# Performance work log

Measured on AMD Instinct MI355X. Metric: run time of the kernel, lower is better.

## Reference

```python
import jax, jax.numpy as jnp
import numpy as np

EMB = 1024
HEADS = 16
HEAD_DIM = EMB // HEADS
EPS = 1e-5


def setup_inputs() -> dict:
    key = jax.random.key(0)
    ks = jax.random.split(key, 10)
    B, T, D = 2, 2048, EMB
    s = 1.0 / np.sqrt(D)
    inp = {
        "x": jax.random.normal(ks[0], (B, T, D), dtype=jnp.float32),
        "wq": jax.random.normal(ks[1], (D, D), dtype=jnp.float32) * s,
        "bq": jnp.zeros((D,), jnp.float32),
        "wk": jax.random.normal(ks[2], (D, D), dtype=jnp.float32) * s,
        "bk": jnp.zeros((D,), jnp.float32),
        "wv": jax.random.normal(ks[3], (D, D), dtype=jnp.float32) * s,
        "bv": jnp.zeros((D,), jnp.float32),
        "wo": jax.random.normal(ks[4], (D, D), dtype=jnp.float32) * s,
        "bo": jnp.zeros((D,), jnp.float32),
        "gamma": jnp.ones((D,), jnp.float32),
        "beta": jnp.zeros((D,), jnp.float32),
    }
    return inp


def _attention(x, wq, bq, wk, bk, wv, bv, wo, bo, gamma, beta):
    B, T, D = x.shape
    H, Hd = HEADS, HEAD_DIM
    q = (x @ wq + bq).reshape(B, T, H, Hd)
    k = (x @ wk + bk).reshape(B, T, H, Hd)
    v = (x @ wv + bv).reshape(B, T, H, Hd)
    # scores: [B, H, T, T]
    scores = jnp.einsum("bthd,bshd->bhts", q, k) / np.sqrt(Hd)
    attn = jax.nn.softmax(scores, axis=-1)  # dropout is identity in eval
    ctx = jnp.einsum("bhts,bshd->bthd", attn, v).reshape(B, T, D)
    out = ctx @ wo + bo
    y = x + out  # residual (dropout identity)
    mu = jnp.mean(y, axis=-1, keepdims=True)
    var = jnp.var(y, axis=-1, keepdims=True)
    return (y - mu) * jax.lax.rsqrt(var + EPS) * gamma + beta


def reference(x, wq, bq, wk, bk, wv, bv, wo, bo, gamma, beta):
    return _attention(x, wq, bq, wk, bk, wv, bv, wo, bo, gamma, beta)
```

## Files before the change

kernel.cpp:

```cpp
#include <hip/hip_runtime.h>

#define BSZ   2
#define TSEQ  2048
#define DMOD  1024
#define NHEAD 16
#define HDIM  64
#define MROW  (BSZ*TSEQ)
#define LNEPS 1e-5f
#define QSCALE 0.18033688011f

typedef __bf16 bf16x8 __attribute__((ext_vector_type(8)));
typedef float  f32x4  __attribute__((ext_vector_type(4)));
typedef unsigned short us8 __attribute__((ext_vector_type(8)));
typedef unsigned short us4 __attribute__((ext_vector_type(4)));

__device__ __forceinline__ unsigned short f2bf(float f) {
    unsigned u = __float_as_uint(f);
    u += 0x7FFF + ((u >> 16) & 1);
    return (unsigned short)(u >> 16);
}
__device__ __forceinline__ float bf2f(unsigned short u) {
    return __uint_as_float((unsigned)u << 16);
}

__device__ __forceinline__ float fexp2(float x) {
#if __has_builtin(__builtin_amdgcn_exp2f)
    return __builtin_amdgcn_exp2f(x);
#else
    return __expf(x * 0.6931471805599453f);
#endif
}

__device__ __forceinline__ void gld_lds16(const void* g, void* l) {
    __builtin_amdgcn_global_load_lds(
        (const __attribute__((address_space(1))) unsigned int*)g,
        (__attribute__((address_space(3))) unsigned int*)l, 16, 0, 0);
}

__global__ __launch_bounds__(256) void prep_k(
    const float* __restrict__ x,
    const float* __restrict__ wq, const float* __restrict__ wk,
    const float* __restrict__ wv, const float* __restrict__ wo,
    unsigned short* __restrict__ Xb,
    unsigned short* __restrict__ WqkvT, unsigned short* __restrict__ WoT)
{
    const int tid = threadIdx.x;
    if (blockIdx.x < 2048) {
        const size_t i = ((size_t)blockIdx.x * 256 + tid) * 8;
        float4 a = *(const float4*)&x[i];
        float4 b = *(const float4*)&x[i + 4];
        union { unsigned short u[8]; uint4 v; } o;
        o.u[0]=f2bf(a.x); o.u[1]=f2bf(a.y); o.u[2]=f2bf(a.z); o.u[3]=f2bf(a.w);
        o.u[4]=f2bf(b.x); o.u[5]=f2bf(b.y); o.u[6]=f2bf(b.z); o.u[7]=f2bf(b.w);
        *(uint4*)&Xb[i] = o.v;
        return;
    }
    __shared__ float T[64][68];
    const int id = blockIdx.x - 2048;
    const int z  = id >> 8;
    const int bx = id & 15;
    const int by = (id >> 4) & 15;
    const float* W = (z == 0) ? wq : (z == 1) ? wk : (z == 2) ? wv : wo;
    unsigned short* Wt = (z < 3) ? (WqkvT + (size_t)z*1024*1024) : WoT;
    const int lr = tid >> 4, lc = (tid & 15) * 4;
    #pragma unroll
    for (int p = 0; p < 4; ++p) {
        const int kk = p*16 + lr;
        float4 v = *(const float4*)&W[(size_t)(by*64 + kk)*1024 + bx*64 + lc];
        T[lc+0][kk] = v.x; T[lc+1][kk] = v.y; T[lc+2][kk] = v.z; T[lc+3][kk] = v.w;
    }
    __syncthreads();
    #pragma unroll
    for (int p = 0; p < 2; ++p) {
        const int nl = p*32 + (tid >> 3);
        const int kb = (tid & 7) * 8;
        float4 a = *(const float4*)&T[nl][kb];
        float4 b = *(const float4*)&T[nl][kb+4];
        union { unsigned short u[8]; uint4 v; } o;
        o.u[0]=f2bf(a.x); o.u[1]=f2bf(a.y); o.u[2]=f2bf(a.z); o.u[3]=f2bf(a.w);
        o.u[4]=f2bf(b.x); o.u[5]=f2bf(b.y); o.u[6]=f2bf(b.z); o.u[7]=f2bf(b.w);
        *(uint4*)&Wt[(size_t)(bx*64 + nl)*1024 + by*64 + kb] = o.v;
    }
}


#define PH_SYNC() do { __builtin_amdgcn_s_barrier(); \
    asm volatile("s_waitcnt lgkmcnt(0)" ::: "memory"); \
    __builtin_amdgcn_sched_barrier(0); } while (0)

template<int N>
__device__ __forceinline__ void vmwait() {
    if constexpr (N == 0)      asm volatile("s_waitcnt vmcnt(0)" ::: "memory");
    else if constexpr (N == 2) asm volatile("s_waitcnt vmcnt(2)" ::: "memory");
    else if constexpr (N == 3) asm volatile("s_waitcnt vmcnt(3)" ::: "memory");
    else                       asm volatile("s_waitcnt vmcnt(4)" ::: "memory");
}

template<int NB>
struct CoreT {
    const unsigned short *sA, *sB;
    unsigned short *A0w, *A1w, *B0w, *B1w;
    const unsigned short *fA0, *fA1, *fB0, *fB1;
    int swz0, swz1;
};

__device__ __forceinline__ void stageA4(const unsigned short* s, unsigned short* d) {
    #pragma unroll
    for (int u = 0; u < 4; ++u) gld_lds16(s + u*64*1024, d + u*4096);
}
template<int NB>
__device__ __forceinline__ void stageBall(const unsigned short* s, unsigned short* d) {
    #pragma unroll
    for (int u = 0; u < NB; ++u) gld_lds16(s + u*64*1024, d + u*4096);
}
__device__ __forceinline__ void stageB01(const unsigned short* s, unsigned short* d) {
    gld_lds16(s, d); gld_lds16(s + 64*1024, d + 4096);
}
template<int NB>
__device__ __forceinline__ void stageBrest(const unsigned short* s, unsigned short* d) {
    #pragma unroll
    for (int u = 2; u < NB; ++u) gld_lds16(s + u*64*1024, d + u*4096);
}

template<int NB>
__device__ __forceinline__ void core_setup(CoreT<NB>& C, unsigned short* LDS,
    const unsigned short* A, const unsigned short* Bt, int bm, int bn, int kbase)
{
    const int tid = threadIdx.x;
    const int w = tid >> 6, lane = tid & 63;
    const int quad = lane >> 4, l16 = lane & 15;
    const int wm = w >> 2, wn = w & 3;
    const int r_l = lane >> 3, c_l = lane & 7;
    C.sA = A  + (size_t)(bm + w*8 + r_l)*1024 + (c_l ^ r_l)*8 + kbase;
    C.sB = Bt + (size_t)(bn + w*8 + r_l)*1024 + (c_l ^ r_l)*8 + kbase;
    unsigned short* A0 = LDS;
    unsigned short* A1 = LDS + 16384;
    unsigned short* B0 = LDS + 32768;
    unsigned short* B1 = B0 + NB*4096;
    C.A0w = A0 + w*512; C.A1w = A1 + w*512;
    C.B0w = B0 + w*512; C.B1w = B1 + w*512;
    C.fA0 = A0 + (wm*128 + l16)*64; C.fA1 = A1 + (wm*128 + l16)*64;
    C.fB0 = B0 + (wn*NB*16 + l16)*64;  C.fB1 = B1 + (wn*NB*16 + l16)*64;
    C.swz0 = ( quad      ^ (l16 & 7)) * 8;
    C.swz1 = ((4 + quad) ^ (l16 & 7)) * 8;
}

template<int NB>
__device__ __forceinline__ void ld_b(const CoreT<NB>& C, bf16x8 (&bfr)[NB][2],
                                     const unsigned short* fB) {
    #pragma unroll
    for (int n = 0; n < NB; ++n) {
        bfr[n][0] = *(const bf16x8*)(fB + n*1024 + C.swz0);
        bfr[n][1] = *(const bf16x8*)(fB + n*1024 + C.swz1);
    }
}

template<int Q, int NB>
__device__ __forceinline__ void ld_a(const CoreT<NB>& C, bf16x8 (&af)[2][2],
                                     const unsigned short* fA) {
    #pragma unroll
    for (int dm = 0; dm < 2; ++dm) {
        af[dm][0] = *(const bf16x8*)(fA + (Q*2+dm)*1024 + C.swz0);
        af[dm][1] = *(const bf16x8*)(fA + (Q*2+dm)*1024 + C.swz1);
    }
}

template<int Q, int NB>
__device__ __forceinline__ void mma_q(f32x4 (&acc)[8][NB], bf16x8 (&af)[2][2],
                                      bf16x8 (&bfr)[NB][2]) {
    __builtin_amdgcn_s_setprio(1);
    #pragma unroll
    for (int dm = 0; dm < 2; ++dm)
        #pragma unroll
        for (int n = 0; n < NB; ++n) {
            f32x4 t = acc[Q*2+dm][n];
            t = __builtin_amdgcn_mfma_f32_16x16x32_bf16(af[dm][0], bfr[n][0], t, 0, 0, 0);
            t = __builtin_amdgcn_mfma_f32_16x16x32_bf16(af[dm][1], bfr[n][1], t, 0, 0, 0);
            acc[Q*2+dm][n] = t;
        }
    __builtin_amdgcn_s_setprio(0);
}

template<int NIT, int NB>
__device__ __forceinline__ void core_kloop(const CoreT<NB>& C, f32x4 (&acc)[8][NB])
{
    stageA4(C.sA, C.A0w);
    stageBall<NB>(C.sB,      C.B0w);
    stageBall<NB>(C.sB + 64, C.B1w);
    vmwait<NB>();
    __builtin_amdgcn_s_barrier();

    bf16x8 bfr[NB][2];
    bf16x8 af[2][2];

    #pragma unroll 1
    for (int it = 0; it < NIT - 1; ++it) {
        const int kk = it * 128;
        ld_b<NB>(C, bfr, C.fB0);
        ld_a<0,NB>(C, af, C.fA0);
        stageA4(C.sA + kk + 64, C.A1w);
        PH_SYNC();  mma_q<0,NB>(acc, af, bfr);
        __builtin_amdgcn_s_barrier();
        ld_a<1,NB>(C, af, C.fA0);
        stageB01(C.sB + kk + 128, C.B0w);
        PH_SYNC();  mma_q<1,NB>(acc, af, bfr);
        __builtin_amdgcn_s_barrier();
        ld_a<2,NB>(C, af, C.fA0);
        stageBrest<NB>(C.sB + kk + 128, C.B0w);
        PH_SYNC();  mma_q<2,NB>(acc, af, bfr);
        __builtin_amdgcn_s_barrier();
        ld_a<3,NB>(C, af, C.fA0);
        PH_SYNC();  mma_q<3,NB>(acc, af, bfr);
        vmwait<NB>();
        __builtin_amdgcn_s_barrier();
        ld_b<NB>(C, bfr, C.fB1);
        ld_a<0,NB>(C, af, C.fA1);
        stageA4(C.sA + kk + 128, C.A0w);
        PH_SYNC();  mma_q<0,NB>(acc, af, bfr);
        __builtin_amdgcn_s_barrier();
        ld_a<1,NB>(C, af, C.fA1);
        stageB01(C.sB + kk + 192, C.B1w);
        PH_SYNC();  mma_q<1,NB>(acc, af, bfr);
        __builtin_amdgcn_s_barrier();
        ld_a<2,NB>(C, af, C.fA1);
        stageBrest<NB>(C.sB + kk + 192, C.B1w);
        PH_SYNC();  mma_q<2,NB>(acc, af, bfr);
        __builtin_amdgcn_s_barrier();
        ld_a<3,NB>(C, af, C.fA1);
        PH_SYNC();  mma_q<3,NB>(acc, af, bfr);
        vmwait<NB>();
        __builtin_amdgcn_s_barrier();
    }

    {
        const int kk = (NIT - 1) * 128;
        ld_b<NB>(C, bfr, C.fB0);
        ld_a<0,NB>(C, af, C.fA0);
        stageA4(C.sA + kk + 64, C.A1w);
        PH_SYNC();  mma_q<0,NB>(acc, af, bfr);
        __builtin_amdgcn_s_barrier();
        ld_a<1,NB>(C, af, C.fA0); PH_SYNC(); mma_q<1,NB>(acc, af, bfr); __builtin_amdgcn_s_barrier();
        ld_a<2,NB>(C, af, C.fA0); PH_SYNC(); mma_q<2,NB>(acc, af, bfr); __builtin_amdgcn_s_barrier();
        ld_a<3,NB>(C, af, C.fA0); PH_SYNC(); mma_q<3,NB>(acc, af, bfr);
        vmwait<0>();
        __builtin_amdgcn_s_barrier();
        ld_b<NB>(C, bfr, C.fB1);
        ld_a<0,NB>(C, af, C.fA1); PH_SYNC(); mma_q<0,NB>(acc, af, bfr); __builtin_amdgcn_s_barrier();
        ld_a<1,NB>(C, af, C.fA1); PH_SYNC(); mma_q<1,NB>(acc, af, bfr); __builtin_amdgcn_s_barrier();
        ld_a<2,NB>(C, af, C.fA1); PH_SYNC(); mma_q<2,NB>(acc, af, bfr); __builtin_amdgcn_s_barrier();
        ld_a<3,NB>(C, af, C.fA1); PH_SYNC(); mma_q<3,NB>(acc, af, bfr);
    }
}

__global__ __launch_bounds__(512, 1) void gemm_qkv_k(
    const unsigned short* __restrict__ A, const unsigned short* __restrict__ Bt,
    const float* __restrict__ b0, const float* __restrict__ b1,
    const float* __restrict__ b2,
    unsigned short* __restrict__ oQ, unsigned short* __restrict__ oK,
    unsigned short* __restrict__ oV)
{
    extern __shared__ unsigned short LDS[];
    const int ob = blockIdx.x;
    const int wg = (ob & 7) * 24 + (ob >> 3);
    const int by = wg / 12, bx = wg - by*12;
    const int bm = by * 256, bn = bx * 256;

    CoreT<4> C;
    core_setup<4>(C, LDS, A, Bt, bm, bn, 0);

    f32x4 acc[8][4];
    #pragma unroll
    for (int i = 0; i < 8; ++i)
        #pragma unroll
        for (int j = 0; j < 4; ++j) acc[i][j] = (f32x4){0.f,0.f,0.f,0.f};

    core_kloop<8,4>(C, acc);

    const int tid = threadIdx.x;
    const int w = tid >> 6, lane = tid & 63;
    const int quad = lane >> 4, l16 = lane & 15;
    const int wm = w >> 2, wn = w & 3;
    const int seg = bn >> 10;
    const int cb  = bn & 1023;
    if (seg < 2) {
        unsigned short* O = (seg == 0) ? oQ : oK;
        const float sc = (seg == 0) ? QSCALE : 1.0f;
        const float* bias = (seg == 0) ? b0 : b1;
        #pragma unroll
        for (int n = 0; n < 4; ++n) {
            const int col = cb + wn*64 + n*16 + l16;
            const float bs = bias[col];
            #pragma unroll
            for (int m = 0; m < 8; ++m)
                #pragma unroll
                for (int r = 0; r < 4; ++r) {
                    const int grow = bm + wm*128 + m*16 + quad*4 + r;
                    O[(size_t)grow*1024 + col] = f2bf((acc[m][n][r] + bs) * sc);
                }
        }
    } else {
        #pragma unroll
        for (int n = 0; n < 4; ++n) {
            const int ch = cb + wn*64 + n*16 + l16;
            const float bs = b2[ch];
            #pragma unroll
            for (int m = 0; m < 8; ++m) {
                const int grow0 = bm + wm*128 + m*16 + quad*4;
                us4 o;
                #pragma unroll
                for (int r = 0; r < 4; ++r) o[r] = f2bf(acc[m][n][r] + bs);
                *(us4*)&oV[(size_t)ch*MROW + grow0] = o;
            }
        }
    }
}

__global__ __launch_bounds__(512, 2) void gemm_proj_k(
    const unsigned short* __restrict__ A, const unsigned short* __restrict__ Bt,
    unsigned short* __restrict__ P)
{
    extern __shared__ unsigned short LDS[];
    const int ob = blockIdx.x;
    const int wg = (ob & 7) * 16 + (ob >> 3);
    const int by = wg >> 3, bx = wg & 7;
    const int kz = blockIdx.y;
    const int bm = by * 256, bn = bx * 128;

    CoreT<2> C;
    core_setup<2>(C, LDS, A, Bt, bm, bn, kz * 512);

    f32x4 acc[8][2];
    #pragma unroll
    for (int i = 0; i < 8; ++i)
        #pragma unroll
        for (int j = 0; j < 2; ++j) acc[i][j] = (f32x4){0.f,0.f,0.f,0.f};

    core_kloop<4,2>(C, acc);

    const int tid = threadIdx.x;
    const int w = tid >> 6, lane = tid & 63;
    const int quad = lane >> 4, l16 = lane & 15;
    const int wm = w >> 2, wn = w & 3;
    unsigned short* O = P + (size_t)kz*MROW*1024;
    #pragma unroll
    for (int n = 0; n < 2; ++n) {
        const int col = bn + wn*32 + n*16 + l16;
        #pragma unroll
        for (int m = 0; m < 8; ++m)
            #pragma unroll
            for (int r = 0; r < 4; ++r) {
                const int grow = bm + wm*128 + m*16 + quad*4 + r;
                O[(size_t)grow*1024 + col] = f2bf(acc[m][n][r]);
            }
    }
}

__global__ __launch_bounds__(256, 4) void attn_k(
    const unsigned short* __restrict__ Qg,
    const unsigned short* __restrict__ Kg,
    const unsigned short* __restrict__ Vtg,
    unsigned short* __restrict__ CTX)
{
    extern __shared__ __align__(16) char lds_raw[];
    unsigned short* Ks = (unsigned short*)lds_raw;
    unsigned short* Vs = (unsigned short*)(lds_raw + 8192);
    unsigned short* Qs = (unsigned short*)lds_raw;
    float* Od = (float*)lds_raw;
    float* Ld = (float*)(lds_raw + 17408);

    const int tid  = threadIdx.x;
    const int wv   = tid >> 6;
    const int lane = tid & 63;
    const int quad = lane >> 4;
    const int l16  = lane & 15;
    const int wq   = wv & 1;
    const int wk   = wv >> 1;

    const int n    = blockIdx.x;
    const int slot = n >> 3;
    const int grp  = (n & 7) + 8 * (slot >> 5);
    const int qx   = slot & 31;
    const int h    = grp >> 1;
    const int b    = grp & 1;
    const int qb   = qx * 64;

    {
        const int r  = tid >> 2;
        const int cb = (tid & 3) * 16;
        const unsigned short* Qrow = Qg + ((size_t)(b*TSEQ + qb + r))*DMOD + h*HDIM + cb;
        *(us8*)&Qs[r*72 + cb]     = *(const us8*)&Qrow[0];
        *(us8*)&Qs[r*72 + cb + 8] = *(const us8*)&Qrow[8];
    }
    __syncthreads();
    bf16x8 qf[2][2];
    #pragma unroll
    for (int nt = 0; nt < 2; ++nt)
        #pragma unroll
        for (int kh = 0; kh < 2; ++kh)
            qf[nt][kh] = *(const bf16x8*)&Qs[(wq*32 + nt*16 + l16)*72 + kh*32 + quad*8];
    __syncthreads();

    const int sr = lane >> 3;
    const int sc = lane & 7;
    const bool isK = (wv < 2);
    const int part = wv & 1;
    const unsigned short* gbase;
    unsigned int goff[4];
    unsigned short* ldst;
    if (isK) {
        gbase = Kg + ((size_t)(b*TSEQ))*DMOD + h*HDIM;
        #pragma unroll
        for (int s = 0; s < 4; ++s) {
            const int R = part*32 + s*8 + sr;
            const int gc = sc ^ ((R ^ (R >> 2)) & 7);
            goff[s] = (unsigned)(R*DMOD + gc*8);
        }
        ldst = Ks + part*2048;
    } else {
        gbase = Vtg + ((size_t)(h*HDIM))*MROW + b*TSEQ;
        #pragma unroll
        for (int s = 0; s < 4; ++s) {
            const int D = part*32 + s*8 + sr;
            const int gc = sc ^ (D & 7);
            goff[s] = (unsigned)(D*MROW + gc*8);
        }
        ldst = Vs + part*2048;
    }
    const size_t gstep = isK ? (size_t)64*DMOD : (size_t)64;

    const int rowA_l = (l16 >> 2)*8 + (l16 & 3);
    const int rA = wk*32 + rowA_l;
    const int rB = rA + 4;
    const int swA = ((rA ^ (rA >> 2)) & 7);
    const int swB = ((rB ^ (rB >> 2)) & 7);
    const unsigned short* kA0 = &Ks[rA*64 + ( quad      ^ swA)*8];
    const unsigned short* kA1 = &Ks[rA*64 + ((4 + quad) ^ swA)*8];
    const unsigned short* kB0 = &Ks[rB*64 + ( quad      ^ swB)*8];
    const unsigned short* kB1 = &Ks[rB*64 + ((4 + quad) ^ swB)*8];
    const unsigned short* vp[4];
    #pragma unroll
    for (int dt = 0; dt < 4; ++dt)
        vp[dt] = &Vs[(dt*16 + l16)*64 + ((wk*4 + quad) ^ (l16 & 7))*8];

    bf16x8 onef;
    { union { unsigned short u[8]; bf16x8 v; } o1;
      #pragma unroll
      for (int i = 0; i < 8; ++i) o1.u[i] = 0x3F80;
      onef = o1.v; }

    f32x4 oacc[4][2];
    f32x4 lacc[2];
    #pragma unroll
    for (int dt = 0; dt < 4; ++dt)
        #pragma unroll
        for (int nt = 0; nt < 2; ++nt) oacc[dt][nt] = (f32x4){0.f,0.f,0.f,0.f};
    lacc[0] = (f32x4){0.f,0.f,0.f,0.f};
    lacc[1] = (f32x4){0.f,0.f,0.f,0.f};

    #pragma unroll 1
    for (int it = 0; it < 32; ++it) {
        __syncthreads();
        #pragma unroll
        for (int s = 0; s < 4; ++s)
            gld_lds16(gbase + (size_t)it*gstep + goff[s], ldst + s*512);
        __syncthreads();

        bf16x8 ka0 = *(const bf16x8*)kA0;
        bf16x8 ka1 = *(const bf16x8*)kA1;
        bf16x8 kb0 = *(const bf16x8*)kB0;
        bf16x8 kb1 = *(const bf16x8*)kB1;
        bf16x8 vf[4];
        #pragma unroll
        for (int dt = 0; dt < 4; ++dt) vf[dt] = *(const bf16x8*)vp[dt];

        bf16x8 pf[2];
        #pragma unroll
        for (int nt = 0; nt < 2; ++nt) {
            f32x4 z = (f32x4){0.f,0.f,0.f,0.f};
            z = __builtin_amdgcn_mfma_f32_16x16x32_bf16(ka0, qf[nt][0], z, 0, 0, 0);
            f32x4 sA = __builtin_amdgcn_mfma_f32_16x16x32_bf16(ka1, qf[nt][1], z, 0, 0, 0);
            f32x4 z2 = (f32x4){0.f,0.f,0.f,0.f};
            z2 = __builtin_amdgcn_mfma_f32_16x16x32_bf16(kb0, qf[nt][0], z2, 0, 0, 0);
            f32x4 sB = __builtin_amdgcn_mfma_f32_16x16x32_bf16(kb1, qf[nt][1], z2, 0, 0, 0);
            float eA[4], eB[4];
            #pragma unroll
            for (int r = 0; r < 4; ++r) { eA[r] = fexp2(sA[r]); eB[r] = fexp2(sB[r]); }
            union { unsigned d[4]; bf16x8 v; } up;
            up.d[0] = __builtin_amdgcn_perm(__float_as_uint(eA[1]), __float_as_uint(eA[0]), 0x07060302);
            up.d[1] = __builtin_amdgcn_perm(__float_as_uint(eA[3]), __float_as_uint(eA[2]), 0x07060302);
            up.d[2] = __builtin_amdgcn_perm(__float_as_uint(eB[1]), __float_as_uint(eB[0]), 0x07060302);
            up.d[3] = __builtin_amdgcn_perm(__float_as_uint(eB[3]), __float_as_uint(eB[2]), 0x07060302);
            pf[nt] = up.v;
        }
        __builtin_amdgcn_s_setprio(1);
        #pragma unroll
        for (int nt = 0; nt < 2; ++nt) {
            lacc[nt] = __builtin_amdgcn_mfma_f32_16x16x32_bf16(onef, pf[nt], lacc[nt], 0, 0, 0);
            #pragma unroll
            for (int dt = 0; dt < 4; ++dt)
                oacc[dt][nt] = __builtin_amdgcn_mfma_f32_16x16x32_bf16(vf[dt], pf[nt], oacc[dt][nt], 0, 0, 0);
        }
        __builtin_amdgcn_s_setprio(0);
    }

    __syncthreads();
    if (wk == 0) {
        float* od = Od + wq*32*68;
        #pragma unroll
        for (int nt = 0; nt < 2; ++nt) {
            #pragma unroll
            for (int dt = 0; dt < 4; ++dt)
                *(f32x4*)&od[(nt*16 + l16)*68 + dt*16 + quad*4] = oacc[dt][nt];
            if (quad == 0) Ld[wq*32 + nt*16 + l16] = lacc[nt][0];
        }
    }
    __syncthreads();
    if (wk == 1) {
        const float* od = Od + wq*32*68;
        #pragma unroll
        for (int nt = 0; nt < 2; ++nt) {
            const float l = Ld[wq*32 + nt*16 + l16] + lacc[nt][0];
            const float inv = 1.f / l;
            const int q = qb + wq*32 + nt*16 + l16;
            unsigned short* crow = CTX + ((size_t)(b*TSEQ + q))*DMOD + h*HDIM;
            #pragma unroll
            for (int dt = 0; dt < 4; ++dt) {
                f32x4 p = *(const f32x4*)&od[(nt*16 + l16)*68 + dt*16 + quad*4];
                us4 o;
                #pragma unroll
                for (int r = 0; r < 4; ++r) o[r] = f2bf((p[r] + oacc[dt][nt][r]) * inv);
                *(us4*)&crow[dt*16 + quad*4] = o;
            }
        }
    }
}

__global__ __launch_bounds__(256) void red_ln_k(
    const float* __restrict__ x, const unsigned short* __restrict__ P,
    const float* __restrict__ bo,
    const float* __restrict__ gamma, const float* __restrict__ beta,
    float* __restrict__ out)
{
    __shared__ float rs[4], rss[4];
    const int row = blockIdx.x;
    const int tid = threadIdx.x;
    const int c = tid * 4;
    const float4 xv = *(const float4*)&x[(size_t)row*DMOD + c];
    const us4 p0 = *(const us4*)&P[(size_t)row*DMOD + c];
    const us4 p1 = *(const us4*)&P[(size_t)(MROW + row)*DMOD + c];
    const float4 bv4 = *(const float4*)&bo[c];
    const float v0 = xv.x + bf2f(p0[0]) + bf2f(p1[0]) + bv4.x;
    const float v1 = xv.y + bf2f(p0[1]) + bf2f(p1[1]) + bv4.y;
    const float v2 = xv.z + bf2f(p0[2]) + bf2f(p1[2]) + bv4.z;
    const float v3 = xv.w + bf2f(p0[3]) + bf2f(p1[3]) + bv4.w;
    float s  = v0 + v1 + v2 + v3;
    float ss = v0*v0 + v1*v1 + v2*v2 + v3*v3;
    #pragma unroll
    for (int o = 32; o > 0; o >>= 1) {
        s  += __shfl_down(s,  o, 64);
        ss += __shfl_down(ss, o, 64);
    }
    if ((tid & 63) == 0) { rs[tid >> 6] = s; rss[tid >> 6] = ss; }
    __syncthreads();
    s  = rs[0] + rs[1] + rs[2] + rs[3];
    ss = rss[0] + rss[1] + rss[2] + rss[3];
    const float mean = s * (1.f/DMOD);
    const float var  = ss * (1.f/DMOD) - mean*mean;
    const float rstd = rsqrtf(var + LNEPS);
    const float4 gv = *(const float4*)&gamma[c];
    const float4 bv = *(const float4*)&beta[c];
    float4 o;
    o.x = (v0 - mean)*rstd*gv.x + bv.x;
    o.y = (v1 - mean)*rstd*gv.y + bv.y;
    o.z = (v2 - mean)*rstd*gv.z + bv.z;
    o.w = (v3 - mean)*rstd*gv.w + bv.w;
    *(float4*)&out[(size_t)row*DMOD + c] = o;
}

extern "C" void kernel_launch(void* const* d_in, const int* in_sizes, int n_in,
                              void* d_out, int out_size, void* d_ws, size_t ws_size,
                              hipStream_t stream) {
    const float* x     = (const float*)d_in[0];
    const float* wq    = (const float*)d_in[1];
    const float* bq    = (const float*)d_in[2];
    const float* wk    = (const float*)d_in[3];
    const float* bk    = (const float*)d_in[4];
    const float* wvp   = (const float*)d_in[5];
    const float* bvp   = (const float*)d_in[6];
    const float* wo    = (const float*)d_in[7];
    const float* bo    = (const float*)d_in[8];
    const float* gamma = (const float*)d_in[9];
    const float* beta  = (const float*)d_in[10];
    float* out = (float*)d_out;

    unsigned short* Xb    = (unsigned short*)d_ws;
    unsigned short* WqkvT = Xb    + (size_t)MROW*DMOD;
    unsigned short* WoT   = WqkvT + (size_t)3072*1024;
    unsigned short* Qb    = WoT   + (size_t)1024*1024;
    unsigned short* Kb    = Qb    + (size_t)MROW*DMOD;
    unsigned short* VtG   = Kb    + (size_t)MROW*DMOD;
    unsigned short* CTXb  = VtG   + (size_t)DMOD*MROW;
    unsigned short* Pp    = CTXb  + (size_t)MROW*DMOD;

    prep_k<<<3072, 256, 0, stream>>>(x, wq, wk, wvp, wo, Xb, WqkvT, WoT);

    gemm_qkv_k<<<dim3(192), 512, 131072, stream>>>(
        Xb, WqkvT, bq, bk, bvp, Qb, Kb, VtG);

    attn_k<<<dim3(1024), 256, 17664, stream>>>(Qb, Kb, VtG, CTXb);

    gemm_proj_k<<<dim3(128, 2), 512, 98304, stream>>>(CTXb, WoT, Pp);

    red_ln_k<<<MROW, 256, 0, stream>>>(x, Pp, bo, gamma, beta, out);
}
```

Measured before the change: 191.4 us.

## Retile QKV GEMM to 256x192 tiles and rebuild projection GEMM with 128x128 tiles

The QKV GEMM moves from 256x256 tiles over 192 blocks to 256x192 tiles over 256 blocks, so the block count better matches the 256 CUs. Because a 192-wide tile can now straddle the Q/K/V boundary, the epilogue picks the output segment for each 16-column fragment. The output-projection GEMM gets a new 4-wave core with 128x128 tiles and its own double-buffered staging schedule, launched as 512 blocks instead of 256. This raises occupancy and reduces tail imbalance, at the cost of less data reuse per tile and more global loads in total.

After: 191.6 us. No clear change (+0.1%).

```diff
diff --git a/kernel.cpp b/kernel.cpp
--- a/kernel.cpp
+++ b/kernel.cpp
@@ -261,34 +261,35 @@
 {
     extern __shared__ unsigned short LDS[];
     const int ob = blockIdx.x;
-    const int wg = (ob & 7) * 24 + (ob >> 3);
-    const int by = wg / 12, bx = wg - by*12;
-    const int bm = by * 256, bn = bx * 256;
-
-    CoreT<4> C;
-    core_setup<4>(C, LDS, A, Bt, bm, bn, 0);
-
-    f32x4 acc[8][4];
+    const int wg = (ob & 7) * 32 + (ob >> 3);
+    const int by = wg >> 4, bx = wg & 15;
+    const int bm = by * 256, bn = bx * 192;
+
+    CoreT<3> C;
+    core_setup<3>(C, LDS, A, Bt, bm, bn, 0);
+
+    f32x4 acc[8][3];
     #pragma unroll
     for (int i = 0; i < 8; ++i)
         #pragma unroll
-        for (int j = 0; j < 4; ++j) acc[i][j] = (f32x4){0.f,0.f,0.f,0.f};
-
-    core_kloop<8,4>(C, acc);
+        for (int j = 0; j < 3; ++j) acc[i][j] = (f32x4){0.f,0.f,0.f,0.f};
+
+    core_kloop<8,3>(C, acc);
 
     const int tid = threadIdx.x;
     const int w = tid >> 6, lane = tid & 63;
     const int quad = lane >> 4, l16 = lane & 15;
     const int wm = w >> 2, wn = w & 3;
-    const int seg = bn >> 10;
-    const int cb  = bn & 1023;
-    if (seg < 2) {
-        unsigned short* O = (seg == 0) ? oQ : oK;
-        const float sc = (seg == 0) ? QSCALE : 1.0f;
-        const float* bias = (seg == 0) ? b0 : b1;
-        #pragma unroll
-        for (int n = 0; n < 4; ++n) {
-            const int col = cb + wn*64 + n*16 + l16;
+    #pragma unroll
+    for (int n = 0; n < 3; ++n) {
+        const int c0  = bn + wn*48 + n*16;
+        const int seg = c0 >> 10;
+        const int cl0 = c0 & 1023;
+        if (seg < 2) {
+            unsigned short* O = (seg == 0) ? oQ : oK;
+            const float sc = (seg == 0) ? QSCALE : 1.0f;
+            const float* bias = (seg == 0) ? b0 : b1;
+            const int col = cl0 + l16;
             const float bs = bias[col];
             #pragma unroll
             for (int m = 0; m < 8; ++m)
@@ -297,11 +298,8 @@
                     const int grow = bm + wm*128 + m*16 + quad*4 + r;
                     O[(size_t)grow*1024 + col] = f2bf((acc[m][n][r] + bs) * sc);
                 }
-        }
-    } else {
-        #pragma unroll
-        for (int n = 0; n < 4; ++n) {
-            const int ch = cb + wn*64 + n*16 + l16;
+        } else {
+            const int ch = cl0 + l16;
             const float bs = b2[ch];
             #pragma unroll
             for (int m = 0; m < 8; ++m) {
@@ -315,41 +313,179 @@
     }
 }
 
-__global__ __launch_bounds__(512, 2) void gemm_proj_k(
-    const unsigned short* __restrict__ A, const unsigned short* __restrict__ Bt,
-    unsigned short* __restrict__ P)
-{
-    extern __shared__ unsigned short LDS[];
-    const int ob = blockIdx.x;
-    const int wg = (ob & 7) * 16 + (ob >> 3);
-    const int by = wg >> 3, bx = wg & 7;
-    const int kz = blockIdx.y;
-    const int bm = by * 256, bn = bx * 128;
-
-    CoreT<2> C;
-    core_setup<2>(C, LDS, A, Bt, bm, bn, kz * 512);
-
-    f32x4 acc[8][2];
-    #pragma unroll
-    for (int i = 0; i < 8; ++i)
-        #pragma unroll
-        for (int j = 0; j < 2; ++j) acc[i][j] = (f32x4){0.f,0.f,0.f,0.f};
-
-    core_kloop<4,2>(C, acc);
-
+struct CoreP {
+    const unsigned short *sA, *sB;
+    unsigned short *A0w, *A1w, *B0w, *B1w;
+    const unsigned short *fA0, *fA1, *fB0, *fB1;
+    int swz0, swz1;
+};
+
+__device__ __forceinline__ void stage4p(const unsigned short* s, unsigned short* d) {
+    #pragma unroll
+    for (int u = 0; u < 4; ++u) gld_lds16(s + u*32*1024, d + u*2048);
+}
+__device__ __forceinline__ void stage01p(const unsigned short* s, unsigned short* d) {
+    gld_lds16(s, d); gld_lds16(s + 32*1024, d + 2048);
+}
+__device__ __forceinline__ void stage23p(const unsigned short* s, unsigned short* d) {
+    gld_lds16(s + 2*32*1024, d + 2*2048); gld_lds16(s + 3*32*1024, d + 3*2048);
+}
+
+__device__ __forceinline__ void corep_setup(CoreP& C, unsigned short* LDS,
+    const unsigned short* A, const unsigned short* Bt, int bm, int bn, int kbase)
+{
     const int tid = threadIdx.x;
     const int w = tid >> 6, lane = tid & 63;
     const int quad = lane >> 4, l16 = lane & 15;
-    const int wm = w >> 2, wn = w & 3;
+    const int wm = w >> 1, wn = w & 1;
+    const int r_l = lane >> 3, c_l = lane & 7;
+    C.sA = A  + (size_t)(bm + w*8 + r_l)*1024 + (c_l ^ r_l)*8 + kbase;
+    C.sB = Bt + (size_t)(bn + w*8 + r_l)*1024 + (c_l ^ r_l)*8 + kbase;
+    unsigned short* A0 = LDS;
+    unsigned short* A1 = LDS + 8192;
+    unsigned short* B0 = LDS + 16384;
+    unsigned short* B1 = LDS + 24576;
+    C.A0w = A0 + w*512; C.A1w = A1 + w*512;
+    C.B0w = B0 + w*512; C.B1w = B1 + w*512;
+    C.fA0 = A0 + (wm*64 + l16)*64; C.fA1 = A1 + (wm*64 + l16)*64;
+    C.fB0 = B0 + (wn*64 + l16)*64; C.fB1 = B1 + (wn*64 + l16)*64;
+    C.swz0 = ( quad      ^ (l16 & 7)) * 8;
+    C.swz1 = ((4 + quad) ^ (l16 & 7)) * 8;
+}
+
+__device__ __forceinline__ void ld_bp(const CoreP& C, bf16x8 (&bfr)[4][2],
+                                      const unsigned short* fB) {
+    #pragma unroll
+    for (int n = 0; n < 4; ++n) {
+        bfr[n][0] = *(const bf16x8*)(fB + n*1024 + C.swz0);
+        bfr[n][1] = *(const bf16x8*)(fB + n*1024 + C.swz1);
+    }
+}
+template<int Q>
+__device__ __forceinline__ void ld_ap(const CoreP& C, bf16x8 (&af)[2],
+                                      const unsigned short* fA) {
+    af[0] = *(const bf16x8*)(fA + Q*1024 + C.swz0);
+    af[1] = *(const bf16x8*)(fA + Q*1024 + C.swz1);
+}
+template<int Q>
+__device__ __forceinline__ void mma_p(f32x4 (&acc)[4][4], bf16x8 (&af)[2],
+                                      bf16x8 (&bfr)[4][2]) {
+    __builtin_amdgcn_s_setprio(1);
+    #pragma unroll
+    for (int n = 0; n < 4; ++n) {
+        f32x4 t = acc[Q][n];
+        t = __builtin_amdgcn_mfma_f32_16x16x32_bf16(af[0], bfr[n][0], t, 0, 0, 0);
+        t = __builtin_amdgcn_mfma_f32_16x16x32_bf16(af[1], bfr[n][1], t, 0, 0, 0);
+        acc[Q][n] = t;
+    }
+    __builtin_amdgcn_s_setprio(0);
+}
+
+template<int NIT>
+__device__ __forceinline__ void corep_kloop(const CoreP& C, f32x4 (&acc)[4][4])
+{
+    stage4p(C.sA, C.A0w);
+    stage4p(C.sB, C.B0w);
+    stage4p(C.sB + 64, C.B1w);
+    vmwait<4>();
+    __builtin_amdgcn_s_barrier();
+
+    bf16x8 bfr[4][2];
+    bf16x8 af[2];
+
+    #pragma unroll 1
+    for (int it = 0; it < NIT - 1; ++it) {
+        const int kk = it * 128;
+        ld_bp(C, bfr, C.fB0);
+        ld_ap<0>(C, af, C.fA0);
+        stage4p(C.sA + kk + 64, C.A1w);
+        PH_SYNC();  mma_p<0>(acc, af, bfr);
+        __builtin_amdgcn_s_barrier();
+        ld_ap<1>(C, af, C.fA0);
+        stage01p(C.sB + kk + 128, C.B0w);
+        PH_SYNC();  mma_p<1>(acc, af, bfr);
+        __builtin_amdgcn_s_barrier();
+        ld_ap<2>(C, af, C.fA0);
+        stage23p(C.sB + kk + 128, C.B0w);
+        PH_SYNC();  mma_p<2>(acc, af, bfr);
+        __builtin_amdgcn_s_barrier();
+        ld_ap<3>(C, af, C.fA0);
+        PH_SYNC();  mma_p<3>(acc, af, bfr);
+        vmwait<4>();
+        __builtin_amdgcn_s_barrier();
+        ld_bp(C, bfr, C.fB1);
+        ld_ap<0>(C, af, C.fA1);
+        stage4p(C.sA + kk + 128, C.A0w);
+        PH_SYNC();  mma_p<0>(acc, af, bfr);
+        __builtin_amdgcn_s_barrier();
+        ld_ap<1>(C, af, C.fA1);
+        stage01p(C.sB + kk + 192, C.B1w);
+        PH_SYNC();  mma_p<1>(acc, af, bfr);
+        __builtin_amdgcn_s_barrier();
+        ld_ap<2>(C, af, C.fA1);
+        stage23p(C.sB + kk + 192, C.B1w);
+        PH_SYNC();  mma_p<2>(acc, af, bfr);
+        __builtin_amdgcn_s_barrier();
+        ld_ap<3>(C, af, C.fA1);
+        PH_SYNC();  mma_p<3>(acc, af, bfr);
+        vmwait<4>();
+        __builtin_amdgcn_s_barrier();
+    }
+    {
+        const int kk = (NIT - 1) * 128;
+        ld_bp(C, bfr, C.fB0);
+        ld_ap<0>(C, af, C.fA0);
+        stage4p(C.sA + kk + 64, C.A1w);
+        PH_SYNC();  mma_p<0>(acc, af, bfr);
+        __builtin_amdgcn_s_barrier();
+        ld_ap<1>(C, af, C.fA0); PH_SYNC(); mma_p<1>(acc, af, bfr); __builtin_amdgcn_s_barrier();
+        ld_ap<2>(C, af, C.fA0); PH_SYNC(); mma_p<2>(acc, af, bfr); __builtin_amdgcn_s_barrier();
+        ld_ap<3>(C, af, C.fA0); PH_SYNC(); mma_p<3>(acc, af, bfr);
+        vmwait<0>();
+        __builtin_amdgcn_s_barrier();
+        ld_bp(C, bfr, C.fB1);
+        ld_ap<0>(C, af, C.fA1); PH_SYNC(); mma_p<0>(acc, af, bfr); __builtin_amdgcn_s_barrier();
+        ld_ap<1>(C, af, C.fA1); PH_SYNC(); mma_p<1>(acc, af, bfr); __builtin_amdgcn_s_barrier();
+        ld_ap<2>(C, af, C.fA1); PH_SYNC(); mma_p<2>(acc, af, bfr); __builtin_amdgcn_s_barrier();
+        ld_ap<3>(C, af, C.fA1); PH_SYNC(); mma_p<3>(acc, af, bfr);
+    }
+}
+
+__global__ __launch_bounds__(256, 2) void gemm_proj_k(
+    const unsigned short* __restrict__ A, const unsigned short* __restrict__ Bt,
+    unsigned short* __restrict__ P)
+{
+    extern __shared__ unsigned short LDS[];
+    const int ob = blockIdx.x;
+    const int wg = (ob & 7) * 32 + (ob >> 3);
+    const int by = wg >> 3, bx = wg & 7;
+    const int kz = blockIdx.y;
+    const int bm = by * 128, bn = bx * 128;
+
+    CoreP C;
+    corep_setup(C, LDS, A, Bt, bm, bn, kz * 512);
+
+    f32x4 acc[4][4];
+    #pragma unroll
+    for (int i = 0; i < 4; ++i)
+        #pragma unroll
+        for (int j = 0; j < 4; ++j) acc[i][j] = (f32x4){0.f,0.f,0.f,0.f};
+
+    corep_kloop<4>(C, acc);
+
+    const int tid = threadIdx.x;
+    const int w = tid >> 6, lane = tid & 63;
+    const int quad = lane >> 4, l16 = lane & 15;
+    const int wm = w >> 1, wn = w & 1;
     unsigned short* O = P + (size_t)kz*MROW*1024;
     #pragma unroll
-    for (int n = 0; n < 2; ++n) {
-        const int col = bn + wn*32 + n*16 + l16;
-        #pragma unroll
-        for (int m = 0; m < 8; ++m)
+    for (int n = 0; n < 4; ++n) {
+        const int col = bn + wn*64 + n*16 + l16;
+        #pragma unroll
+        for (int m = 0; m < 4; ++m)
             #pragma unroll
             for (int r = 0; r < 4; ++r) {
-                const int grow = bm + wm*128 + m*16 + quad*4 + r;
+                const int grow = bm + wm*64 + m*16 + quad*4 + r;
                 O[(size_t)grow*1024 + col] = f2bf(acc[m][n][r]);
             }
     }
@@ -604,12 +740,12 @@
 
     prep_k<<<3072, 256, 0, stream>>>(x, wq, wk, wvp, wo, Xb, WqkvT, WoT);
 
-    gemm_qkv_k<<<dim3(192), 512, 131072, stream>>>(
+    gemm_qkv_k<<<dim3(256), 512, 114688, stream>>>(
         Xb, WqkvT, bq, bk, bvp, Qb, Kb, VtG);
 
     attn_k<<<dim3(1024), 256, 17664, stream>>>(Qb, Kb, VtG, CTXb);
 
-    gemm_proj_k<<<dim3(128, 2), 512, 98304, stream>>>(CTXb, WoT, Pp);
+    gemm_proj_k<<<dim3(256, 2), 256, 65536, stream>>>(CTXb, WoT, Pp);
 
     red_ln_k<<<MROW, 256, 0, stream>>>(x, Pp, bo, gamma, beta, out);
 }
```

## Retile QKV GEMM to 256x192 blocks and double attention KV tile

Applied to the files above, without the earlier changes.

The QKV projection GEMM now uses 256x192 output tiles, giving 256 workgroups instead of 192 to fill the CUs more evenly. Because a 192-wide tile can cross the Q/K/V boundaries, the epilogue now picks the destination per 16-column group. The attention kernel loads 128 keys per iteration instead of 64, halving the loop count and the barriers per key, with a new V swizzle for the 128-wide rows. The cost is more LDS per attention block, which could lower occupancy, and a tile shape that may load the MFMA less evenly.

New measurement: 200.6 us. +4.8%, slower.

```diff
diff --git a/kernel.cpp b/kernel.cpp
--- a/kernel.cpp
+++ b/kernel.cpp
@@ -82,7 +82,6 @@
         *(uint4*)&Wt[(size_t)(bx*64 + nl)*1024 + by*64 + kb] = o.v;
     }
 }
-
 
 #define PH_SYNC() do { __builtin_amdgcn_s_barrier(); \
     asm volatile("s_waitcnt lgkmcnt(0)" ::: "memory"); \
@@ -231,7 +230,6 @@
         vmwait<NB>();
         __builtin_amdgcn_s_barrier();
     }
-
     {
         const int kk = (NIT - 1) * 128;
         ld_b<NB>(C, bfr, C.fB0);
@@ -261,34 +259,35 @@
 {
     extern __shared__ unsigned short LDS[];
     const int ob = blockIdx.x;
-    const int wg = (ob & 7) * 24 + (ob >> 3);
-    const int by = wg / 12, bx = wg - by*12;
-    const int bm = by * 256, bn = bx * 256;
-
-    CoreT<4> C;
-    core_setup<4>(C, LDS, A, Bt, bm, bn, 0);
-
-    f32x4 acc[8][4];
+    const int wg = (ob & 7) * 32 + (ob >> 3);
+    const int by = wg >> 4, bx = wg & 15;
+    const int bm = by * 256, bn = bx * 192;
+
+    CoreT<3> C;
+    core_setup<3>(C, LDS, A, Bt, bm, bn, 0);
+
+    f32x4 acc[8][3];
     #pragma unroll
     for (int i = 0; i < 8; ++i)
         #pragma unroll
-        for (int j = 0; j < 4; ++j) acc[i][j] = (f32x4){0.f,0.f,0.f,0.f};
-
-    core_kloop<8,4>(C, acc);
+        for (int j = 0; j < 3; ++j) acc[i][j] = (f32x4){0.f,0.f,0.f,0.f};
+
+    core_kloop<8,3>(C, acc);
 
     const int tid = threadIdx.x;
     const int w = tid >> 6, lane = tid & 63;
     const int quad = lane >> 4, l16 = lane & 15;
     const int wm = w >> 2, wn = w & 3;
-    const int seg = bn >> 10;
-    const int cb  = bn & 1023;
-    if (seg < 2) {
-        unsigned short* O = (seg == 0) ? oQ : oK;
-        const float sc = (seg == 0) ? QSCALE : 1.0f;
-        const float* bias = (seg == 0) ? b0 : b1;
-        #pragma unroll
-        for (int n = 0; n < 4; ++n) {
-            const int col = cb + wn*64 + n*16 + l16;
+    #pragma unroll
+    for (int n = 0; n < 3; ++n) {
+        const int c0  = bn + wn*48 + n*16;
+        const int seg = c0 >> 10;
+        const int cl0 = c0 & 1023;
+        if (seg < 2) {
+            unsigned short* O = (seg == 0) ? oQ : oK;
+            const float sc = (seg == 0) ? QSCALE : 1.0f;
+            const float* bias = (seg == 0) ? b0 : b1;
+            const int col = cl0 + l16;
             const float bs = bias[col];
             #pragma unroll
             for (int m = 0; m < 8; ++m)
@@ -297,11 +296,8 @@
                     const int grow = bm + wm*128 + m*16 + quad*4 + r;
                     O[(size_t)grow*1024 + col] = f2bf((acc[m][n][r] + bs) * sc);
                 }
-        }
-    } else {
-        #pragma unroll
-        for (int n = 0; n < 4; ++n) {
-            const int ch = cb + wn*64 + n*16 + l16;
+        } else {
+            const int ch = cl0 + l16;
             const float bs = b2[ch];
             #pragma unroll
             for (int m = 0; m < 8; ++m) {
@@ -363,10 +359,10 @@
 {
     extern __shared__ __align__(16) char lds_raw[];
     unsigned short* Ks = (unsigned short*)lds_raw;
-    unsigned short* Vs = (unsigned short*)(lds_raw + 8192);
+    unsigned short* Vs = (unsigned short*)(lds_raw + 16384);
     unsigned short* Qs = (unsigned short*)lds_raw;
     float* Od = (float*)lds_raw;
-    float* Ld = (float*)(lds_raw + 17408);
+    float* Ld = (float*)(lds_raw + 32768);
 
     const int tid  = threadIdx.x;
     const int wv   = tid >> 6;
@@ -400,47 +396,52 @@
             qf[nt][kh] = *(const bf16x8*)&Qs[(wq*32 + nt*16 + l16)*72 + kh*32 + quad*8];
     __syncthreads();
 
-    const int sr = lane >> 3;
-    const int sc = lane & 7;
     const bool isK = (wv < 2);
     const int part = wv & 1;
     const unsigned short* gbase;
-    unsigned int goff[4];
+    unsigned int goff[8];
     unsigned short* ldst;
     if (isK) {
+        const int sr = lane >> 3, sc = lane & 7;
         gbase = Kg + ((size_t)(b*TSEQ))*DMOD + h*HDIM;
         #pragma unroll
-        for (int s = 0; s < 4; ++s) {
-            const int R = part*32 + s*8 + sr;
+        for (int s = 0; s < 8; ++s) {
+            const int R = part*64 + s*8 + sr;
             const int gc = sc ^ ((R ^ (R >> 2)) & 7);
             goff[s] = (unsigned)(R*DMOD + gc*8);
         }
-        ldst = Ks + part*2048;
+        ldst = Ks + part*4096;
     } else {
+        const int vr = lane >> 4;
+        const int cl = lane & 15;
         gbase = Vtg + ((size_t)(h*HDIM))*MROW + b*TSEQ;
         #pragma unroll
-        for (int s = 0; s < 4; ++s) {
-            const int D = part*32 + s*8 + sr;
-            const int gc = sc ^ (D & 7);
-            goff[s] = (unsigned)(D*MROW + gc*8);
+        for (int s = 0; s < 8; ++s) {
+            const int d = part*32 + s*4 + vr;
+            const int gc = cl ^ (d & 15);
+            goff[s] = (unsigned)(d*MROW + gc*8);
         }
-        ldst = Vs + part*2048;
-    }
-    const size_t gstep = isK ? (size_t)64*DMOD : (size_t)64;
+        ldst = Vs + part*4096;
+    }
+    const size_t gstep = isK ? (size_t)128*DMOD : (size_t)128;
 
     const int rowA_l = (l16 >> 2)*8 + (l16 & 3);
-    const int rA = wk*32 + rowA_l;
-    const int rB = rA + 4;
-    const int swA = ((rA ^ (rA >> 2)) & 7);
-    const int swB = ((rB ^ (rB >> 2)) & 7);
-    const unsigned short* kA0 = &Ks[rA*64 + ( quad      ^ swA)*8];
-    const unsigned short* kA1 = &Ks[rA*64 + ((4 + quad) ^ swA)*8];
-    const unsigned short* kB0 = &Ks[rB*64 + ( quad      ^ swB)*8];
-    const unsigned short* kB1 = &Ks[rB*64 + ((4 + quad) ^ swB)*8];
-    const unsigned short* vp[4];
-    #pragma unroll
-    for (int dt = 0; dt < 4; ++dt)
-        vp[dt] = &Vs[(dt*16 + l16)*64 + ((wk*4 + quad) ^ (l16 & 7))*8];
+    const unsigned short* kp[2][4];
+    const unsigned short* vp[2][4];
+    #pragma unroll
+    for (int g = 0; g < 2; ++g) {
+        const int rA = wk*64 + g*32 + rowA_l;
+        const int rB = rA + 4;
+        const int swA = (rA ^ (rA >> 2)) & 7;
+        const int swB = (rB ^ (rB >> 2)) & 7;
+        kp[g][0] = &Ks[rA*64 + (( quad      ^ swA))*8];
+        kp[g][1] = &Ks[rA*64 + (((4 + quad) ^ swA))*8];
+        kp[g][2] = &Ks[rB*64 + (( quad      ^ swB))*8];
+        kp[g][3] = &Ks[rB*64 + (((4 + quad) ^ swB))*8];
+        #pragma unroll
+        for (int dt = 0; dt < 4; ++dt)
+            vp[g][dt] = &Vs[(dt*16 + l16)*128 + (((wk*8 + g*4 + quad) ^ l16))*8];
+    }
 
     bf16x8 onef;
     { union { unsigned short u[8]; bf16x8 v; } o1;
@@ -458,49 +459,52 @@
     lacc[1] = (f32x4){0.f,0.f,0.f,0.f};
 
     #pragma unroll 1
-    for (int it = 0; it < 32; ++it) {
+    for (int it = 0; it < 16; ++it) {
         __syncthreads();
         #pragma unroll
-        for (int s = 0; s < 4; ++s)
+        for (int s = 0; s < 8; ++s)
             gld_lds16(gbase + (size_t)it*gstep + goff[s], ldst + s*512);
         __syncthreads();
 
-        bf16x8 ka0 = *(const bf16x8*)kA0;
-        bf16x8 ka1 = *(const bf16x8*)kA1;
-        bf16x8 kb0 = *(const bf16x8*)kB0;
-        bf16x8 kb1 = *(const bf16x8*)kB1;
-        bf16x8 vf[4];
-        #pragma unroll
-        for (int dt = 0; dt < 4; ++dt) vf[dt] = *(const bf16x8*)vp[dt];
-
-        bf16x8 pf[2];
-        #pragma unroll
-        for (int nt = 0; nt < 2; ++nt) {
-            f32x4 z = (f32x4){0.f,0.f,0.f,0.f};
-            z = __builtin_amdgcn_mfma_f32_16x16x32_bf16(ka0, qf[nt][0], z, 0, 0, 0);
-            f32x4 sA = __builtin_amdgcn_mfma_f32_16x16x32_bf16(ka1, qf[nt][1], z, 0, 0, 0);
-            f32x4 z2 = (f32x4){0.f,0.f,0.f,0.f};
-            z2 = __builtin_amdgcn_mfma_f32_16x16x32_bf16(kb0, qf[nt][0], z2, 0, 0, 0);
-            f32x4 sB = __builtin_amdgcn_mfma_f32_16x16x32_bf16(kb1, qf[nt][1], z2, 0, 0, 0);
-            float eA[4], eB[4];
-            #pragma unroll
-            for (int r = 0; r < 4; ++r) { eA[r] = fexp2(sA[r]); eB[r] = fexp2(sB[r]); }
-            union { unsigned d[4]; bf16x8 v; } up;
-            up.d[0] = __builtin_amdgcn_perm(__float_as_uint(eA[1]), __float_as_uint(eA[0]), 0x07060302);
-            up.d[1] = __builtin_amdgcn_perm(__float_as_uint(eA[3]), __float_as_uint(eA[2]), 0x07060302);
-            up.d[2] = __builtin_amdgcn_perm(__float_as_uint(eB[1]), __float_as_uint(eB[0]), 0x07060302);
-            up.d[3] = __builtin_amdgcn_perm(__float_as_uint(eB[3]), __float_as_uint(eB[2]), 0x07060302);
-            pf[nt] = up.v;
+        #pragma unroll
+        for (int g = 0; g < 2; ++g) {
+            bf16x8 ka0 = *(const bf16x8*)kp[g][0];
+            bf16x8 ka1 = *(const bf16x8*)kp[g][1];
+            bf16x8 kb0 = *(const bf16x8*)kp[g][2];
+            bf16x8 kb1 = *(const bf16x8*)kp[g][3];
+            bf16x8 vf[4];
+            #pragma unroll
+            for (int dt = 0; dt < 4; ++dt) vf[dt] = *(const bf16x8*)vp[g][dt];
+
+            bf16x8 pf[2];
+            #pragma unroll
+            for (int nt = 0; nt < 2; ++nt) {
+                f32x4 z = (f32x4){0.f,0.f,0.f,0.f};
+                z = __builtin_amdgcn_mfma_f32_16x16x32_bf16(ka0, qf[nt][0], z, 0, 0, 0);
+                f32x4 sA = __builtin_amdgcn_mfma_f32_16x16x32_bf16(ka1, qf[nt][1], z, 0, 0, 0);
+                f32x4 z2 = (f32x4){0.f,0.f,0.f,0.f};
+                z2 = __builtin_amdgcn_mfma_f32_16x16x32_bf16(kb0, qf[nt][0], z2, 0, 0, 0);
+                f32x4 sB = __builtin_amdgcn_mfma_f32_16x16x32_bf16(kb1, qf[nt][1], z2, 0, 0, 0);
+                float eA[4], eB[4];
+                #pragma unroll
+                for (int r = 0; r < 4; ++r) { eA[r] = fexp2(sA[r]); eB[r] = fexp2(sB[r]); }
+                union { unsigned d[4]; bf16x8 v; } up;
+                up.d[0] = __builtin_amdgcn_perm(__float_as_uint(eA[1]), __float_as_uint(eA[0]), 0x07060302);
+                up.d[1] = __builtin_amdgcn_perm(__float_as_uint(eA[3]), __float_as_uint(eA[2]), 0x07060302);
+                up.d[2] = __builtin_amdgcn_perm(__float_as_uint(eB[1]), __float_as_uint(eB[0]), 0x07060302);
+                up.d[3] = __builtin_amdgcn_perm(__float_as_uint(eB[3]), __float_as_uint(eB[2]), 0x07060302);
+                pf[nt] = up.v;
+            }
+            __builtin_amdgcn_s_setprio(1);
+            #pragma unroll
+            for (int nt = 0; nt < 2; ++nt) {
+                lacc[nt] = __builtin_amdgcn_mfma_f32_16x16x32_bf16(onef, pf[nt], lacc[nt], 0, 0, 0);
+                #pragma unroll
+                for (int dt = 0; dt < 4; ++dt)
+                    oacc[dt][nt] = __builtin_amdgcn_mfma_f32_16x16x32_bf16(vf[dt], pf[nt], oacc[dt][nt], 0, 0, 0);
+            }
+            __builtin_amdgcn_s_setprio(0);
         }
-        __builtin_amdgcn_s_setprio(1);
-        #pragma unroll
-        for (int nt = 0; nt < 2; ++nt) {
-            lacc[nt] = __builtin_amdgcn_mfma_f32_16x16x32_bf16(onef, pf[nt], lacc[nt], 0, 0, 0);
-            #pragma unroll
-            for (int dt = 0; dt < 4; ++dt)
-                oacc[dt][nt] = __builtin_amdgcn_mfma_f32_16x16x32_bf16(vf[dt], pf[nt], oacc[dt][nt], 0, 0, 0);
-        }
-        __builtin_amdgcn_s_setprio(0);
     }
 
     __syncthreads();
@@ -604,10 +608,10 @@
 
     prep_k<<<3072, 256, 0, stream>>>(x, wq, wk, wvp, wo, Xb, WqkvT, WoT);
 
-    gemm_qkv_k<<<dim3(192), 512, 131072, stream>>>(
+    gemm_qkv_k<<<dim3(256), 512, 114688, stream>>>(
         Xb, WqkvT, bq, bk, bvp, Qb, Kb, VtG);
 
-    attn_k<<<dim3(1024), 256, 17664, stream>>>(Qb, Kb, VtG, CTXb);
+    attn_k<<<dim3(1024), 256, 33024, stream>>>(Qb, Kb, VtG, CTXb);
 
     gemm_proj_k<<<dim3(128, 2), 512, 98304, stream>>>(CTXb, WoT, Pp);
 
```
